# Kernel tuning notes

Measured on AMD Instinct MI355X. Metric: run time of the kernel, lower is better.

The kernel has to match this reference:

```python
import jax, jax.numpy as jnp
import numpy as np

N_HEADS, N_LEVELS, N_POINTS = 8, 4, 4
D_MODEL, D_FFN = 256, 2048
NQ, BS = 900, 4
SPATIAL = np.array([[128, 128], [64, 64], [32, 32], [16, 16]], dtype=np.int64)
HW = int((SPATIAL[:, 0] * SPATIAL[:, 1]).sum())


def _ln(x, g, b):
    mu = x.mean(-1, keepdims=True)
    var = x.var(-1, keepdims=True)
    return (x - mu) / jnp.sqrt(var + 1e-5) * g + b


def _lin(x, w, b):
    return x @ w.T + b


def _msdeform_attn(query, refp, mem, ss, starts, so_w, so_b, aw_w, aw_b, vp_w, vp_b, op_w, op_b):
    # query: (bs, nq, d), refp: (bs, nq, L, 2) in [0,1], mem: (bs, hw, d)
    bs, nq, d = query.shape
    hd = d // N_HEADS
    value = _lin(mem, vp_w, vp_b).reshape(bs, -1, N_HEADS, hd)  # (bs, hw, H, hd)
    offsets = _lin(query, so_w, so_b).reshape(bs, nq, N_HEADS, N_LEVELS, N_POINTS, 2)
    aw = _lin(query, aw_w, aw_b).reshape(bs, nq, N_HEADS, N_LEVELS * N_POINTS)
    aw = jax.nn.softmax(aw, axis=-1).reshape(bs, nq, N_HEADS, N_LEVELS, N_POINTS)
    # offset normalizer is (W, H) per level
    normalizer = jnp.asarray(ss[:, ::-1].copy(), dtype=query.dtype)  # (L, 2)
    loc = refp[:, :, None, :, None, :] + offsets / normalizer[None, None, None, :, None, :]
    out = jnp.zeros((bs, nq, N_HEADS, hd), dtype=query.dtype)
    for l in range(N_LEVELS):
        h_l, w_l = int(ss[l, 0]), int(ss[l, 1])
        vl = value[:, starts[l]:starts[l] + h_l * w_l]  # (bs, h*w, H, hd)
        # grid_sample align_corners=False: pixel coord = loc*size - 0.5
        x = loc[:, :, :, l, :, 0] * w_l - 0.5  # (bs, nq, H, P)
        y = loc[:, :, :, l, :, 1] * h_l - 0.5
        x0 = jnp.floor(x)
        y0 = jnp.floor(y)
        fx = x - x0
        fy = y - y0

        def gather(ix, iy, wgt):
            valid = (ix >= 0) & (ix < w_l) & (iy >= 0) & (iy < h_l)
            idx = (jnp.clip(iy, 0, h_l - 1) * w_l + jnp.clip(ix, 0, w_l - 1)).astype(jnp.int32)
            # (bs, nq, H, P) -> (bs, nq*P, H) to match vl's (bs, hw, H, hd)
            idxt = idx.transpose(0, 1, 3, 2).reshape(bs, nq * N_POINTS, N_HEADS)
            g = jnp.take_along_axis(vl, idxt[..., None], axis=1)  # (bs, nq*P, H, hd)
            g = g.reshape(bs, nq, N_POINTS, N_HEADS, hd).transpose(0, 1, 3, 2, 4)
            return g * (wgt * valid)[..., None]

        x0i = x0.astype(jnp.int32)
        y0i = y0.astype(jnp.int32)
        sampled = (gather(x0i, y0i, (1 - fx) * (1 - fy))
                   + gather(x0i + 1, y0i, fx * (1 - fy))
                   + gather(x0i, y0i + 1, (1 - fx) * fy)
                   + gather(x0i + 1, y0i + 1, fx * fy))  # (bs, nq, H, P, hd)
        out = out + (sampled * aw[:, :, :, l, :, None]).sum(axis=3)
    return _lin(out.reshape(bs, nq, d), op_w, op_b)


def _fwd(tgt, query_pos, memory, ref_points,
         sa_in_w, sa_in_b, sa_out_w, sa_out_b,
         ln1_g, ln1_b, ln2_g, ln2_b, ln3_g, ln3_b,
         so_w, so_b, aw_w, aw_b, vp_w, vp_b, op_w, op_b,
         ff1_w, ff1_b, ff2_w, ff2_b, spatial_shapes, level_start_index):
    nq, bs, d = tgt.shape
    hd = d // N_HEADS
    ss = np.asarray(spatial_shapes)
    starts = np.asarray(level_start_index)
    # ---- self attention (q = k = tgt + pos, v = tgt) ----
    qk = tgt + query_pos
    q = _lin(qk, sa_in_w[:d], sa_in_b[:d]).reshape(nq, bs, N_HEADS, hd)
    k = _lin(qk, sa_in_w[d:2 * d], sa_in_b[d:2 * d]).reshape(nq, bs, N_HEADS, hd)
    v = _lin(tgt, sa_in_w[2 * d:], sa_in_b[2 * d:]).reshape(nq, bs, N_HEADS, hd)
    scores = jnp.einsum('qbhd,kbhd->bhqk', q, k) / np.sqrt(hd).astype(tgt.dtype)
    attn = jax.nn.softmax(scores, axis=-1)
    sa = jnp.einsum('bhqk,kbhd->qbhd', attn, v).reshape(nq, bs, d)
    sa = _lin(sa, sa_out_w, sa_out_b)
    tgt = _ln(tgt + sa, ln2_g, ln2_b)
    # ---- deformable cross attention ----
    ca = _msdeform_attn((tgt + query_pos).transpose(1, 0, 2),
                        ref_points.transpose(1, 0, 2, 3),
                        memory.transpose(1, 0, 2), ss, starts,
                        so_w, so_b, aw_w, aw_b, vp_w, vp_b, op_w, op_b)
    tgt = _ln(tgt + ca.transpose(1, 0, 2), ln1_g, ln1_b)
    # ---- FFN ----
    ff = _lin(jax.nn.relu(_lin(tgt, ff1_w, ff1_b)), ff2_w, ff2_b)
    return _ln(tgt + ff, ln3_g, ln3_b)


def setup_inputs() -> dict:
    key = jax.random.key(0)
    ks = iter(jax.random.split(key, 32))
    d, dffn = D_MODEL, D_FFN
    nofs = N_HEADS * N_LEVELS * N_POINTS
    w = lambda *s: jax.random.normal(next(ks), s, dtype=jnp.float32) * 0.02
    starts = np.concatenate([[0], np.cumsum(SPATIAL[:, 0] * SPATIAL[:, 1])[:-1]]).astype(np.int64)
    return {
        'tgt': jax.random.normal(next(ks), (NQ, BS, d), dtype=jnp.float32),
        'query_pos': jax.random.normal(next(ks), (NQ, BS, d), dtype=jnp.float32),
        'memory': jax.random.normal(next(ks), (HW, BS, d), dtype=jnp.float32),
        'ref_points': jax.random.uniform(next(ks), (NQ, BS, N_LEVELS, 2), dtype=jnp.float32),
        'sa_in_w': w(3 * d, d), 'sa_in_b': w(3 * d), 'sa_out_w': w(d, d), 'sa_out_b': w(d),
        'ln1_g': jnp.ones((d,)), 'ln1_b': jnp.zeros((d,)),
        'ln2_g': jnp.ones((d,)), 'ln2_b': jnp.zeros((d,)),
        'ln3_g': jnp.ones((d,)), 'ln3_b': jnp.zeros((d,)),
        'so_w': w(nofs * 2, d), 'so_b': jax.random.normal(next(ks), (nofs * 2,), dtype=jnp.float32) * 0.5,
        'aw_w': w(nofs, d), 'aw_b': w(nofs),
        'vp_w': w(d, d), 'vp_b': w(d), 'op_w': w(d, d), 'op_b': w(d),
        'ff1_w': w(dffn, d), 'ff1_b': w(dffn), 'ff2_w': w(d, dffn), 'ff2_b': w(d),
        'spatial_shapes': SPATIAL, 'level_start_index': starts,
    }


def reference(tgt, query_pos, memory, ref_points, sa_in_w, sa_in_b, sa_out_w, sa_out_b, ln1_g, ln1_b, ln2_g, ln2_b, ln3_g, ln3_b, so_w, so_b, aw_w, aw_b, vp_w, vp_b, op_w, op_b, ff1_w, ff1_b, ff2_w, ff2_b, spatial_shapes, level_start_index):
    return _fwd(tgt, query_pos, memory, ref_points, sa_in_w, sa_in_b, sa_out_w, sa_out_b,
                ln1_g, ln1_b, ln2_g, ln2_b, ln3_g, ln3_b, so_w, so_b, aw_w, aw_b,
                vp_w, vp_b, op_w, op_b, ff1_w, ff1_b, ff2_w, ff2_b,
                spatial_shapes, level_start_index)
```

## Files before the change

### kernel.cpp

```cpp
#include <hip/hip_runtime.h>
#include <hip/hip_bf16.h>

#define D_MODEL 256
#define N_HEADS 8
#define HD 32
#define NQ 900
#define BS 4
#define MROWS (NQ * BS)
#define HW_TOT 21760
#define VROWS (HW_TOT * BS)

typedef __attribute__((ext_vector_type(8))) short bf16x8;
typedef __attribute__((ext_vector_type(4))) float f32x4;

__device__ inline short f2b(float f) {
  union { __hip_bfloat16 h; short s; } u;
  u.h = __float2bfloat16(f);
  return u.s;
}
__device__ inline float bu2f(unsigned short u) {
  union { unsigned int i; float f; } c;
  c.i = ((unsigned int)u) << 16;
  return c.f;
}
__device__ inline bf16x8 bzero8() {
  bf16x8 v;
#pragma unroll
  for (int j = 0; j < 8; ++j) v[j] = 0;
  return v;
}
__device__ inline f32x4 fzero4() {
  f32x4 v;
#pragma unroll
  for (int j = 0; j < 4; ++j) v[j] = 0.f;
  return v;
}

#define GLL16(gsrc, ldst)                                                     \
  __builtin_amdgcn_global_load_lds(                                           \
      (__attribute__((address_space(1))) void*)(gsrc),                        \
      (__attribute__((address_space(3))) void*)(ldst), 16, 0, 0)

__global__ __launch_bounds__(256) void prep_all(const float* __restrict__ s0,
                                                const float* __restrict__ s1,
                                                const float* __restrict__ s2,
                                                const float* __restrict__ s3,
                                                const float* __restrict__ s4,
                                                const float* __restrict__ s5,
                                                const float* __restrict__ s6,
                                                const float* __restrict__ s7,
                                                short* __restrict__ dst,
                                                const float* __restrict__ tgt,
                                                const float* __restrict__ qpos,
                                                short* __restrict__ tgtb,
                                                short* __restrict__ qkb,
                                                const float* __restrict__ so_b,
                                                const float* __restrict__ aw_b,
                                                float* __restrict__ biasSOAW) {
  int i = blockIdx.x * 256 + threadIdx.x;
  if (i < 1540096) {
    const float* s; int off;
    if (i < 196608)      { s = s0; off = 0; }
    else if (i < 262144) { s = s1; off = 196608; }
    else if (i < 327680) { s = s2; off = 262144; }
    else if (i < 360448) { s = s3; off = 327680; }
    else if (i < 425984) { s = s4; off = 360448; }
    else if (i < 491520) { s = s5; off = 425984; }
    else if (i < 1015808){ s = s6; off = 491520; }
    else                 { s = s7; off = 1015808; }
    dst[i] = f2b(s[i - off]);
  } else {
    int j = i - 1540096;
    float t = tgt[j], p = qpos[j];
    tgtb[j] = f2b(t);
    qkb[j] = f2b(t + p);
    if (j < 384) biasSOAW[j] = (j < 256) ? so_b[j] : aw_b[j - 256];
  }
}

template <int BN, int AF32, int OUTF32, int RELU>
__device__ __forceinline__ void gemm_core(const void* __restrict__ Xv,
                                          const short* __restrict__ W,
                                          const float* __restrict__ bias,
                                          void* __restrict__ outv,
                                          int M, int N, int K, int m0, int n0,
                                          int t0, int t1, int addBias,
                                          short* __restrict__ smem) {
  constexpr int NF = BN / 16;
  short* sA = smem;
  short* sB = smem + 2 * 2048;
  const int tid = threadIdx.x;
  const int wave = tid >> 6, lane = tid & 63;
  const int l15 = lane & 15, l4 = lane >> 4;
  const int wr = wave * 16;
  const float* Xf = (const float*)Xv;
  const short* Xh = (const short*)Xv;

  f32x4 acc[NF];
#pragma unroll
  for (int f = 0; f < NF; ++f) acc[f] = fzero4();

  const int alr = wave * 16 + (lane >> 2);
  const int ags = (lane & 3) ^ ((alr >> 1) & 3);
  const int arow = tid >> 2, ak = tid & 3;
  const int agsrc = ak ^ ((arow >> 1) & 3);
  float4 ra0, ra1;

  auto stageB = [&](int t, int buf) {
    short* bb = sB + buf * BN * 32;
#pragma unroll
    for (int j = 0; j < BN / 64; ++j) {
      int lr = j * 64 + alr;
      int gs = (lane & 3) ^ ((lr >> 1) & 3);
      const short* src = W + (size_t)(n0 + lr) * K + t * 32 + gs * 8;
      GLL16(src, bb + (j * 64 + wave * 16) * 32);
    }
  };
  auto stageA_gll = [&](int t, int buf) {
    const short* src = Xh + (size_t)(m0 + alr) * K + t * 32 + ags * 8;
    GLL16(src, sA + buf * 2048 + wave * 512);
  };
  auto loadA_f32 = [&](int t) {
    const float* p = Xf + (size_t)(m0 + arow) * K + t * 32 + agsrc * 8;
    ra0 = *reinterpret_cast<const float4*>(p);
    ra1 = *reinterpret_cast<const float4*>(p + 4);
  };
  auto writeA_f32 = [&](int buf) {
    bf16x8 v;
    v[0] = f2b(ra0.x); v[1] = f2b(ra0.y); v[2] = f2b(ra0.z); v[3] = f2b(ra0.w);
    v[4] = f2b(ra1.x); v[5] = f2b(ra1.y); v[6] = f2b(ra1.z); v[7] = f2b(ra1.w);
    *reinterpret_cast<bf16x8*>(&sA[buf * 2048 + arow * 32 + ak * 8]) = v;
  };
  auto compute = [&](int buf) {
    const int r = wr + l15;
    bf16x8 av = *reinterpret_cast<const bf16x8*>(
        &sA[buf * 2048 + r * 32 + ((l4 ^ ((r >> 1) & 3)) * 8)]);
#pragma unroll
    for (int f = 0; f < NF; ++f) {
      const int rb = f * 16 + l15;
      bf16x8 bv = *reinterpret_cast<const bf16x8*>(
          &sB[buf * BN * 32 + rb * 32 + ((l4 ^ ((rb >> 1) & 3)) * 8)]);
      acc[f] = __builtin_amdgcn_mfma_f32_16x16x32_bf16(av, bv, acc[f], 0, 0, 0);
    }
  };

  if constexpr (AF32) { loadA_f32(t0); writeA_f32(0); }
  else stageA_gll(t0, 0);
  stageB(t0, 0);
  __syncthreads();

  int buf = 0;
  for (int t = t0; t < t1; ++t) {
    if (t + 1 < t1) {
      if constexpr (AF32) loadA_f32(t + 1);
      else stageA_gll(t + 1, buf ^ 1);
      stageB(t + 1, buf ^ 1);
    }
    compute(buf);
    if (AF32 && t + 1 < t1) writeA_f32(buf ^ 1);
    __syncthreads();
    buf ^= 1;
  }

#pragma unroll
  for (int f = 0; f < NF; ++f) {
    int col = n0 + f * 16 + l15;
    float bfv = addBias ? bias[col] : 0.f;
#pragma unroll
    for (int i = 0; i < 4; ++i) {
      int row = m0 + wr + l4 * 4 + i;
      if (row >= M) continue;
      float v = acc[f][i] + bfv;
      if (RELU) v = fmaxf(v, 0.f);
      if constexpr (OUTF32)
        ((float*)outv)[(size_t)row * N + col] = v;
      else
        ((short*)outv)[(size_t)row * N + col] = f2b(v);
    }
  }
}

template <int BN, int AF32, int OUTF32, int RELU>
__global__ __launch_bounds__(256) void gemm2(const void* __restrict__ Xv,
                                             const short* __restrict__ W,
                                             const float* __restrict__ bias,
                                             void* __restrict__ outv,
                                             int M, int N, int K) {
  __shared__ __align__(16) short smem[2 * 2048 + 2 * BN * 32];
  gemm_core<BN, AF32, OUTF32, RELU>(Xv, W, bias, outv, M, N, K,
                                    blockIdx.x * 64, blockIdx.y * BN,
                                    0, K / 32, 1, smem);
}

__global__ __launch_bounds__(256) void gemm_splitk(const void* __restrict__ Xv,
                                                   const short* __restrict__ W,
                                                   const float* __restrict__ bias,
                                                   float* __restrict__ outp,
                                                   int M, int N, int K) {
  __shared__ __align__(16) short smem[2 * 2048 + 2 * 64 * 32];
  const int kc = blockIdx.z;
  const int ntc = K / 32 / 4;
  gemm_core<64, 0, 1, 0>(Xv, W, bias, outp + (size_t)kc * M * N, M, N, K,
                         blockIdx.x * 64, blockIdx.y * 64,
                         kc * ntc, (kc + 1) * ntc, kc == 0, smem);
}

__global__ __launch_bounds__(256) void qkv_gemm(const short* __restrict__ qkb,
                                                const short* __restrict__ tgtb,
                                                const short* __restrict__ Wqkv,
                                                const float* __restrict__ sa_in_b,
                                                short* __restrict__ QKb,
                                                short* __restrict__ Vb) {
  __shared__ __align__(16) short smem[2 * 2048 + 2 * 64 * 32];
  int bx = blockIdx.x;
  if (bx < 456) {
    gemm_core<64, 0, 0, 0>(qkb, Wqkv, sa_in_b, QKb, MROWS, 512, 256,
                           (bx % 57) * 64, (bx / 57) * 64, 0, 8, 1, smem);
  } else {
    bx -= 456;
    gemm_core<64, 0, 0, 0>(tgtb, Wqkv + 512 * 256, sa_in_b + 512, Vb, MROWS, 256, 256,
                           (bx % 57) * 64, (bx / 57) * 64, 0, 8, 1, smem);
  }
}

__device__ __forceinline__ void flash_body(const short* __restrict__ QK,
                                           const short* __restrict__ V,
                                           short* __restrict__ O,
                                           int bid, short* __restrict__ smem) {
  const int bh = bid & 31, b = bh >> 3, h = bh & 7;
  const int q0 = (bid >> 5) * 64;
  const int tid = threadIdx.x, wave = tid >> 6, lane = tid & 63;
  const int l15 = lane & 15, l4 = lane >> 4;
  const int cb = h * 32;

  short* sQ = smem;
  short* sK = smem + 2048;
  short* sVt = smem + 6144;
  short* sP = smem + 10752;

  const int sr = wave * 16 + (lane >> 2);
  const int sgs = (lane & 3) ^ (sr & 3);

  auto stageK = [&](int kt, int buf) {
    const short* src = QK + (size_t)((kt * 64 + sr) * 4 + b) * 512 + 256 + cb + sgs * 8;
    GLL16(src, sK + buf * 2048 + wave * 512);
  };
  const int vrow = tid >> 2, vdof = (tid & 3) * 8;
  const int vkp = vrow ^ (((vdof >> 3) & 3) << 4);
  auto loadV = [&](int kt) -> bf16x8 {
    int kk = kt * 64 + vrow;
    return (kk < NQ)
        ? *reinterpret_cast<const bf16x8*>(V + (size_t)(kk * 4 + b) * 256 + cb + vdof)
        : bzero8();
  };
  auto writeV = [&](bf16x8 vv, int buf) {
    short* dst = sVt + buf * 2304;
#pragma unroll
    for (int j = 0; j < 8; ++j) dst[(vdof + j) * 72 + vkp] = vv[j];
  };

  {
    const short* qsrc = QK + (size_t)((q0 + sr) * 4 + b) * 512 + cb + sgs * 8;
    GLL16(qsrc, sQ + wave * 512);
  }
  stageK(0, 0);
  {
    bf16x8 v0 = loadV(0);
    writeV(v0, 0);
  }
  __syncthreads();

  const int wr = wave * 16;
  const int rq = wr + l15;
  const bf16x8 aq = *reinterpret_cast<const bf16x8*>(&sQ[rq * 32 + ((l4 ^ (rq & 3)) * 8)]);

  float mrow[4], lrow[4];
#pragma unroll
  for (int i = 0; i < 4; ++i) { mrow[i] = -1e30f; lrow[i] = 0.f; }
  f32x4 accO[2];
  accO[0] = fzero4(); accO[1] = fzero4();

  const int pswz = (((wr >> 2) + l4) & 3) << 3;
  const int pswzr = (((wr >> 2) + (l15 >> 2)) & 3) << 3;

  for (int kt = 0; kt < 15; ++kt) {
    const int k0 = kt * 64;
    const int buf = kt & 1;
    const bool more = (kt + 1 < 15);
    bf16x8 vnext = bzero8();
    if (more) {
      stageK(kt + 1, buf ^ 1);
      vnext = loadV(kt + 1);
    }

    f32x4 s[4];
#pragma unroll
    for (int f = 0; f < 4; ++f) {
      const int rb = f * 16 + l15;
      bf16x8 bk = *reinterpret_cast<bf16x8*>(
          &sK[buf * 2048 + rb * 32 + ((l4 ^ (rb & 3)) * 8)]);
      s[f] = __builtin_amdgcn_mfma_f32_16x16x32_bf16(aq, bk, fzero4(), 0, 0, 0);
    }
#pragma unroll
    for (int f = 0; f < 4; ++f) {
      bool valid = (k0 + f * 16 + l15) < NQ;
#pragma unroll
      for (int i = 0; i < 4; ++i) {
        float sv = s[f][i] * 0.17677669529663687f;
        s[f][i] = valid ? sv : -1e30f;
      }
    }
    float mx[4];
#pragma unroll
    for (int i = 0; i < 4; ++i)
      mx[i] = fmaxf(fmaxf(s[0][i], s[1][i]), fmaxf(s[2][i], s[3][i]));
#pragma unroll
    for (int off = 1; off < 16; off <<= 1)
#pragma unroll
      for (int i = 0; i < 4; ++i) mx[i] = fmaxf(mx[i], __shfl_xor(mx[i], off));

    float alpha[4], rs[4];
#pragma unroll
    for (int i = 0; i < 4; ++i) {
      float mn = fmaxf(mrow[i], mx[i]);
      alpha[i] = __expf(mrow[i] - mn);
      mrow[i] = mn;
      rs[i] = 0.f;
    }
#pragma unroll
    for (int f = 0; f < 4; ++f)
#pragma unroll
      for (int i = 0; i < 4; ++i) {
        float p = __expf(s[f][i] - mrow[i]);
        rs[i] += p;
        sP[(wr + l4 * 4 + i) * 72 + ((f * 16 + l15) ^ pswz)] = f2b(p);
      }
#pragma unroll
    for (int off = 1; off < 16; off <<= 1)
#pragma unroll
      for (int i = 0; i < 4; ++i) rs[i] += __shfl_xor(rs[i], off);
#pragma unroll
    for (int i = 0; i < 4; ++i) lrow[i] = lrow[i] * alpha[i] + rs[i];
#pragma unroll
    for (int nf = 0; nf < 2; ++nf)
#pragma unroll
      for (int i = 0; i < 4; ++i) accO[nf][i] *= alpha[i];

#pragma unroll
    for (int ks = 0; ks < 2; ++ks) {
      bf16x8 ap = *reinterpret_cast<bf16x8*>(
          &sP[(wr + l15) * 72 + ((ks * 32 + l4 * 8) ^ pswzr)]);
#pragma unroll
      for (int nf = 0; nf < 2; ++nf) {
        const int d = nf * 16 + l15;
        const int kb = (ks * 32 + l4 * 8) ^ (((d >> 3) & 3) << 4);
        bf16x8 bv = *reinterpret_cast<bf16x8*>(&sVt[buf * 2304 + d * 72 + kb]);
        accO[nf] = __builtin_amdgcn_mfma_f32_16x16x32_bf16(ap, bv, accO[nf], 0, 0, 0);
      }
    }
    if (more) writeV(vnext, buf ^ 1);
    __syncthreads();
  }

#pragma unroll
  for (int nf = 0; nf < 2; ++nf)
#pragma unroll
    for (int i = 0; i < 4; ++i) {
      int q = q0 + wr + l4 * 4 + i;
      if (q < NQ)
        O[(size_t)(q * 4 + b) * 256 + cb + nf * 16 + l15] = f2b(accO[nf][i] / lrow[i]);
    }
}

__device__ __forceinline__ void value_core(const float* __restrict__ memory,
                                           const short* __restrict__ W,
                                           const float* __restrict__ vp_b,
                                           short* __restrict__ value, int vb,
                                           short* __restrict__ smem) {
  float* sAf = (float*)smem;
  short* sB = smem + 8192;
  const int tid = threadIdx.x;
  const int wave = tid >> 6, lane = tid & 63;
  const int l15 = lane & 15, l4 = lane >> 4;
  const int wr = wave * 16;
  const int m0 = (((vb >> 4) << 3) | (vb & 7)) * 64;
  const int n0 = ((vb >> 3) & 1) * 128;

  const int ar0 = wave * 16 + (lane >> 3);
  const int ag = (lane & 7) ^ (lane >> 3);
  auto stageA = [&](int t, int buf) {
    const float* s0 = memory + (size_t)(m0 + ar0) * 256 + t * 32 + ag * 4;
    GLL16(s0, (short*)sAf + buf * 4096 + wave * 1024);
    const float* s1 = memory + (size_t)(m0 + ar0 + 8) * 256 + t * 32 + ag * 4;
    GLL16(s1, (short*)sAf + buf * 4096 + wave * 1024 + 512);
  };
  const int blr = wave * 16 + (lane >> 2);
  auto stageB = [&](int t, int buf) {
#pragma unroll
    for (int j = 0; j < 2; ++j) {
      int lr = j * 64 + blr;
      int gs = (lane & 3) ^ ((lr >> 1) & 3);
      const short* src = W + (size_t)(n0 + lr) * 256 + t * 32 + gs * 8;
      GLL16(src, sB + buf * 4096 + (j * 64 + wave * 16) * 32);
    }
  };

  f32x4 acc[8];
#pragma unroll
  for (int f = 0; f < 8; ++f) acc[f] = fzero4();

  auto compute = [&](int buf) {
    const int r = wr + l15;
    const int rx = r & 7;
    const float* ap = sAf + buf * 2048 + r * 32;
    float4 a0 = *reinterpret_cast<const float4*>(ap + (((2 * l4) ^ rx) * 4));
    float4 a1 = *reinterpret_cast<const float4*>(ap + (((2 * l4 + 1) ^ rx) * 4));
    bf16x8 av;
    av[0] = f2b(a0.x); av[1] = f2b(a0.y); av[2] = f2b(a0.z); av[3] = f2b(a0.w);
    av[4] = f2b(a1.x); av[5] = f2b(a1.y); av[6] = f2b(a1.z); av[7] = f2b(a1.w);
#pragma unroll
    for (int f = 0; f < 8; ++f) {
      const int rb = f * 16 + l15;
      bf16x8 bv = *reinterpret_cast<const bf16x8*>(
          &sB[buf * 4096 + rb * 32 + ((l4 ^ ((rb >> 1) & 3)) * 8)]);
      acc[f] = __builtin_amdgcn_mfma_f32_16x16x32_bf16(av, bv, acc[f], 0, 0, 0);
    }
  };

  stageA(0, 0); stageB(0, 0);
  stageA(1, 1); stageB(1, 1);
  asm volatile("s_waitcnt vmcnt(4)" ::: "memory");
  __builtin_amdgcn_sched_barrier(0);
  __builtin_amdgcn_s_barrier();
  __builtin_amdgcn_sched_barrier(0);

#pragma unroll
  for (int t = 0; t < 8; ++t) {
    const int buf = t & 1;
    compute(buf);
    asm volatile("s_waitcnt lgkmcnt(0)" ::: "memory");
    __builtin_amdgcn_sched_barrier(0);
    __builtin_amdgcn_s_barrier();
    __builtin_amdgcn_sched_barrier(0);
    if (t + 2 < 8) { stageA(t + 2, buf); stageB(t + 2, buf); }
    if (t + 1 < 8) {
      if (t + 2 < 8) asm volatile("s_waitcnt vmcnt(4)" ::: "memory");
      else           asm volatile("s_waitcnt vmcnt(0)" ::: "memory");
      __builtin_amdgcn_sched_barrier(0);
      __builtin_amdgcn_s_barrier();
      __builtin_amdgcn_sched_barrier(0);
    }
  }

#pragma unroll
  for (int f = 0; f < 8; ++f) {
    const int col = n0 + f * 16 + l15;
    const float bb = vp_b[col];
#pragma unroll
    for (int i = 0; i < 4; ++i)
      value[(size_t)(m0 + wr + l4 * 4 + i) * 256 + col] = f2b(acc[f][i] + bb);
  }
}

__global__ __launch_bounds__(256) void flash_value(const short* __restrict__ QKb,
                                                   const short* __restrict__ Vb,
                                                   short* __restrict__ Ob,
                                                   const float* __restrict__ memory,
                                                   const short* __restrict__ Wvp,
                                                   const float* __restrict__ vp_b,
                                                   short* __restrict__ value) {
  __shared__ __align__(16) short smem[16384];
  int bx = blockIdx.x;
  if (bx < 480) {
    flash_body(QKb, Vb, Ob, bx, smem);
  } else {
    value_core(memory, Wvp, vp_b, value, bx - 480, smem);
  }
}

__global__ __launch_bounds__(256) void ln_kernel(const float* __restrict__ A,
                                                 const float* __restrict__ B,
                                                 const float* __restrict__ g,
                                                 const float* __restrict__ bb,
                                                 float* __restrict__ outF,
                                                 short* __restrict__ outB,
                                                 const float* __restrict__ addv) {
  const int row = blockIdx.x;
  const int t = threadIdx.x;
  const size_t base = (size_t)row * D_MODEL;
  float x = A[base + t] + B[base + t];
  float s = x, s2 = x * x;
#pragma unroll
  for (int off = 32; off; off >>= 1) {
    s += __shfl_xor(s, off);
    s2 += __shfl_xor(s2, off);
  }
  __shared__ float wsum[4], wsum2[4];
  const int w = t >> 6;
  if ((t & 63) == 0) { wsum[w] = s; wsum2[w] = s2; }
  __syncthreads();
  s = wsum[0] + wsum[1] + wsum[2] + wsum[3];
  s2 = wsum2[0] + wsum2[1] + wsum2[2] + wsum2[3];
  const float mu = s * (1.f / 256.f);
  const float var = s2 * (1.f / 256.f) - mu * mu;
  const float inv = rsqrtf(var + 1e-5f);
  float y = (x - mu) * inv * g[t] + bb[t];
  outF[base + t] = y;
  if (outB) outB[base + t] = f2b(y + (addv ? addv[base + t] : 0.f));
}

__global__ __launch_bounds__(256) void ln4_kernel(const float* __restrict__ A,
                                                  const float* __restrict__ P,
                                                  const float* __restrict__ g,
                                                  const float* __restrict__ bb,
                                                  float* __restrict__ outF) {
  const int row = blockIdx.x;
  const int t = threadIdx.x;
  const size_t base = (size_t)row * D_MODEL + t;
  const size_t stride = (size_t)MROWS * D_MODEL;
  float x = A[base] + P[base] + P[base + stride] + P[base + 2 * stride] + P[base + 3 * stride];
  float s = x, s2 = x * x;
#pragma unroll
  for (int off = 32; off; off >>= 1) {
    s += __shfl_xor(s, off);
    s2 += __shfl_xor(s2, off);
  }
  __shared__ float wsum[4], wsum2[4];
  const int w = t >> 6;
  if ((t & 63) == 0) { wsum[w] = s; wsum2[w] = s2; }
  __syncthreads();
  s = wsum[0] + wsum[1] + wsum[2] + wsum[3];
  s2 = wsum2[0] + wsum2[1] + wsum2[2] + wsum2[3];
  const float mu = s * (1.f / 256.f);
  const float var = s2 * (1.f / 256.f) - mu * mu;
  const float inv = rsqrtf(var + 1e-5f);
  outF[base] = (x - mu) * inv * g[t] + bb[t];
}

__global__ __launch_bounds__(256) void msds_kernel(const unsigned short* __restrict__ value,
                                                   const float* __restrict__ soaw,
                                                   const float* __restrict__ refp,
                                                   unsigned short* __restrict__ out) {
  const int tid = threadIdx.x;
  const int row = blockIdx.x * 8 + (tid >> 5);
  const int lane32 = tid & 31;
  const int h = lane32 >> 2;
  const int dp = (lane32 & 3) * 8;
  const int b = row & 3;

  const int WL[4] = {128, 64, 32, 16};
  const int ST[4] = {0, 16384, 20480, 21504};

  const float* awp = soaw + (size_t)row * 384 + 256 + h * 16;
  float awv[16];
  float m = -1e30f;
#pragma unroll
  for (int i = 0; i < 16; ++i) { awv[i] = awp[i]; m = fmaxf(m, awv[i]); }
  float s = 0.f;
#pragma unroll
  for (int i = 0; i < 16; ++i) { awv[i] = __expf(awv[i] - m); s += awv[i]; }
  const float invs = 1.f / s;

  const float* offp = soaw + (size_t)row * 384 + h * 32;
  float acc[8];
#pragma unroll
  for (int j = 0; j < 8; ++j) acc[j] = 0.f;

#pragma unroll
  for (int l = 0; l < 4; ++l) {
    const int wl = WL[l], hl = WL[l], st = ST[l];
    const float rx = refp[((size_t)row * 4 + l) * 2 + 0];
    const float ry = refp[((size_t)row * 4 + l) * 2 + 1];
#pragma unroll
    for (int p = 0; p < 4; ++p) {
      const float ox = offp[l * 8 + p * 2 + 0];
      const float oy = offp[l * 8 + p * 2 + 1];
      const float x = (rx + ox / (float)wl) * (float)wl - 0.5f;
      const float y = (ry + oy / (float)hl) * (float)hl - 0.5f;
      const float x0f = floorf(x), y0f = floorf(y);
      const int x0 = (int)x0f, y0 = (int)y0f;
      const float fx = x - x0f, fy = y - y0f;
      const float a = awv[l * 4 + p] * invs;
      const float w00 = (1.f - fx) * (1.f - fy);
      const float w10 = fx * (1.f - fy);
      const float w01 = (1.f - fx) * fy;
      const float w11 = fx * fy;
      float sv[8];
#pragma unroll
      for (int j = 0; j < 8; ++j) sv[j] = 0.f;
      auto gat = [&](int ix, int iy, float wgt) {
        if (ix >= 0 && ix < wl && iy >= 0 && iy < hl) {
          const unsigned short* p2 =
              value + ((size_t)((st + iy * wl + ix) * 4 + b)) * 256 + h * 32 + dp;
          bf16x8 u = *reinterpret_cast<const bf16x8*>(p2);
#pragma unroll
          for (int j = 0; j < 8; ++j) sv[j] += wgt * bu2f((unsigned short)u[j]);
        }
      };
      gat(x0, y0, w00);
      gat(x0 + 1, y0, w10);
      gat(x0, y0 + 1, w01);
      gat(x0 + 1, y0 + 1, w11);
#pragma unroll
      for (int j = 0; j < 8; ++j) acc[j] += a * sv[j];
    }
  }
  bf16x8 o;
#pragma unroll
  for (int j = 0; j < 8; ++j) o[j] = f2b(acc[j]);
  *reinterpret_cast<bf16x8*>(&out[(size_t)row * 256 + h * 32 + dp]) = o;
}

extern "C" void kernel_launch(void* const* d_in, const int* in_sizes, int n_in,
                              void* d_out, int out_size, void* d_ws, size_t ws_size,
                              hipStream_t stream) {
  const float* tgt      = (const float*)d_in[0];
  const float* qpos     = (const float*)d_in[1];
  const float* memory   = (const float*)d_in[2];
  const float* refp     = (const float*)d_in[3];
  const float* sa_in_w  = (const float*)d_in[4];
  const float* sa_in_b  = (const float*)d_in[5];
  const float* sa_out_w = (const float*)d_in[6];
  const float* sa_out_b = (const float*)d_in[7];
  const float* ln1_g = (const float*)d_in[8];
  const float* ln1_b = (const float*)d_in[9];
  const float* ln2_g = (const float*)d_in[10];
  const float* ln2_b = (const float*)d_in[11];
  const float* ln3_g = (const float*)d_in[12];
  const float* ln3_b = (const float*)d_in[13];
  const float* so_w = (const float*)d_in[14];
  const float* so_b = (const float*)d_in[15];
  const float* aw_w = (const float*)d_in[16];
  const float* aw_b = (const float*)d_in[17];
  const float* vp_w = (const float*)d_in[18];
  const float* vp_b = (const float*)d_in[19];
  const float* op_w = (const float*)d_in[20];
  const float* op_b = (const float*)d_in[21];
  const float* ff1_w = (const float*)d_in[22];
  const float* ff1_b = (const float*)d_in[23];
  const float* ff2_w = (const float*)d_in[24];
  const float* ff2_b = (const float*)d_in[25];

  float* out = (float*)d_out;
  float* ws = (float*)d_ws;

  short* Wb       = (short*)ws;
  float* biasSOAW = ws + 770048;
  short* tgtb   = (short*)(ws + 770432);
  short* qkb    = (short*)(ws + 1231232);
  short* QKb    = (short*)(ws + 1692032);
  short* Vb     = (short*)(ws + 2613632);
  short* Ob     = (short*)(ws + 3074432);
  float* SA     = ws + 3535232;
  float* F      = ws + 4456832;
  short* qk2b   = (short*)(ws + 5378432);
  float* SOAW   = ws + 5839232;
  short* value  = (short*)(ws + 7221632);
  short* sampled= (short*)(ws + 18362752);
  float* CA     = ws + 18823552;
  float* tgt3   = ws + 19745152;
  short* tgt3b  = (short*)(ws + 20666752);
  short* H      = (short*)(ws + 21127552);
  float* FFp    = ws + 7221632;

  const short* Wqkv = Wb;
  const short* Wsa  = Wb + 196608;
  const short* Wso  = Wb + 262144;
  const short* Wvp  = Wb + 360448;
  const short* Wop  = Wb + 425984;
  const short* Wff1 = Wb + 491520;
  const short* Wff2 = Wb + 1015808;

  prep_all<<<9616, 256, 0, stream>>>(sa_in_w, sa_out_w, so_w, aw_w, vp_w, op_w,
                                     ff1_w, ff2_w, Wb, tgt, qpos, tgtb, qkb,
                                     so_b, aw_b, biasSOAW);
  qkv_gemm<<<684, 256, 0, stream>>>(qkb, tgtb, Wqkv, sa_in_b, QKb, Vb);
  flash_value<<<3200, 256, 0, stream>>>(QKb, Vb, Ob, memory, Wvp, vp_b, value);
  gemm2<64, 0, 1, 0><<<dim3(57, 4), 256, 0, stream>>>(Ob, Wsa, sa_out_b, SA, MROWS, 256, 256);
  ln_kernel<<<MROWS, 256, 0, stream>>>(tgt, SA, ln2_g, ln2_b, F, qk2b, qpos);
  gemm2<64, 0, 1, 0><<<dim3(57, 6), 256, 0, stream>>>(qk2b, Wso, biasSOAW, SOAW, MROWS, 384, 256);
  msds_kernel<<<450, 256, 0, stream>>>((const unsigned short*)value, SOAW, refp,
                                       (unsigned short*)sampled);
  gemm2<64, 0, 1, 0><<<dim3(57, 4), 256, 0, stream>>>(sampled, Wop, op_b, CA, MROWS, 256, 256);
  ln_kernel<<<MROWS, 256, 0, stream>>>(F, CA, ln1_g, ln1_b, tgt3, tgt3b, nullptr);
  gemm2<64, 0, 0, 1><<<dim3(57, 32), 256, 0, stream>>>(tgt3b, Wff1, ff1_b, H, MROWS, 2048, 256);
  gemm_splitk<<<dim3(57, 4, 4), 256, 0, stream>>>(H, Wff2, ff2_b, FFp, MROWS, 256, 2048);
  ln4_kernel<<<MROWS, 256, 0, stream>>>(tgt3, FFp, ln3_g, ln3_b, out);
}
```

Baseline: 161.4 us.

## Fuse output-projection GEMMs with residual LayerNorm; triple-buffer value projection

Adds a gemm_ln kernel that computes a full 256-column row tile per block, adds bias and residual, and applies LayerNorm in registers. It replaces the two gemm2 + ln_kernel pairs, which removes two launches and the fp32 intermediate round trips through global memory. The cost is a grid of only 57 blocks, so most CUs sit idle during these GEMMs. Separately, the value-projection path in flash_value now uses three pipeline stages instead of two, which raises shared memory per block to 48KB and may lower occupancy for the flash blocks.

New measurement: 195.4 us. 21.1% more time.

```diff
diff --git a/kernel.cpp b/kernel.cpp
--- a/kernel.cpp
+++ b/kernel.cpp
@@ -205,6 +205,113 @@
                          kc * ntc, (kc + 1) * ntc, kc == 0, smem);
 }
 
+__global__ __launch_bounds__(256) void gemm_ln(const short* __restrict__ X,
+                                               const short* __restrict__ W,
+                                               const float* __restrict__ bias,
+                                               const float* __restrict__ R,
+                                               const float* __restrict__ g,
+                                               const float* __restrict__ bvec,
+                                               float* __restrict__ outF,
+                                               short* __restrict__ outB,
+                                               const float* __restrict__ addv) {
+  __shared__ __align__(16) short smem[2 * 2048 + 2 * 8192];
+  short* sA = smem;
+  short* sB = smem + 2 * 2048;
+  const int tid = threadIdx.x;
+  const int wave = tid >> 6, lane = tid & 63;
+  const int l15 = lane & 15, l4 = lane >> 4;
+  const int wr = wave * 16;
+  const int m0 = blockIdx.x * 64;
+
+  f32x4 acc[16];
+#pragma unroll
+  for (int f = 0; f < 16; ++f) acc[f] = fzero4();
+
+  const int alr = wave * 16 + (lane >> 2);
+  const int ags = (lane & 3) ^ ((alr >> 1) & 3);
+
+  auto stageA = [&](int t, int buf) {
+    const short* src = X + (size_t)(m0 + alr) * 256 + t * 32 + ags * 8;
+    GLL16(src, sA + buf * 2048 + wave * 512);
+  };
+  auto stageB = [&](int t, int buf) {
+#pragma unroll
+    for (int j = 0; j < 4; ++j) {
+      int lr = j * 64 + alr;
+      int gs = (lane & 3) ^ ((lr >> 1) & 3);
+      const short* src = W + (size_t)lr * 256 + t * 32 + gs * 8;
+      GLL16(src, sB + buf * 8192 + (j * 64 + wave * 16) * 32);
+    }
+  };
+  auto compute = [&](int buf) {
+    const int r = wr + l15;
+    bf16x8 av = *reinterpret_cast<const bf16x8*>(
+        &sA[buf * 2048 + r * 32 + ((l4 ^ ((r >> 1) & 3)) * 8)]);
+#pragma unroll
+    for (int f = 0; f < 16; ++f) {
+      const int rb = f * 16 + l15;
+      bf16x8 bv = *reinterpret_cast<const bf16x8*>(
+          &sB[buf * 8192 + rb * 32 + ((l4 ^ ((rb >> 1) & 3)) * 8)]);
+      acc[f] = __builtin_amdgcn_mfma_f32_16x16x32_bf16(av, bv, acc[f], 0, 0, 0);
+    }
+  };
+
+  stageA(0, 0); stageB(0, 0);
+  __syncthreads();
+  int buf = 0;
+  for (int t = 0; t < 8; ++t) {
+    if (t + 1 < 8) { stageA(t + 1, buf ^ 1); stageB(t + 1, buf ^ 1); }
+    compute(buf);
+    __syncthreads();
+    buf ^= 1;
+  }
+
+  float sum[4] = {0.f, 0.f, 0.f, 0.f}, sum2[4] = {0.f, 0.f, 0.f, 0.f};
+#pragma unroll
+  for (int f = 0; f < 16; ++f) {
+    const int col = f * 16 + l15;
+    const float bc = bias[col];
+#pragma unroll
+    for (int i = 0; i < 4; ++i) {
+      const int row = m0 + wr + l4 * 4 + i;
+      float r = (row < MROWS) ? R[(size_t)row * 256 + col] : 0.f;
+      float v = acc[f][i] + bc + r;
+      acc[f][i] = v;
+      sum[i] += v;
+      sum2[i] += v * v;
+    }
+  }
+#pragma unroll
+  for (int off = 1; off < 16; off <<= 1)
+#pragma unroll
+    for (int i = 0; i < 4; ++i) {
+      sum[i] += __shfl_xor(sum[i], off);
+      sum2[i] += __shfl_xor(sum2[i], off);
+    }
+  float mu[4], inv[4];
+#pragma unroll
+  for (int i = 0; i < 4; ++i) {
+    mu[i] = sum[i] * (1.f / 256.f);
+    float var = sum2[i] * (1.f / 256.f) - mu[i] * mu[i];
+    inv[i] = rsqrtf(var + 1e-5f);
+  }
+#pragma unroll
+  for (int f = 0; f < 16; ++f) {
+    const int col = f * 16 + l15;
+    const float gc = g[col], bc = bvec[col];
+#pragma unroll
+    for (int i = 0; i < 4; ++i) {
+      const int row = m0 + wr + l4 * 4 + i;
+      if (row >= MROWS) continue;
+      float y = (acc[f][i] - mu[i]) * inv[i] * gc + bc;
+      outF[(size_t)row * 256 + col] = y;
+      if (outB)
+        outB[(size_t)row * 256 + col] =
+            f2b(y + (addv ? addv[(size_t)row * 256 + col] : 0.f));
+    }
+  }
+}
+
 __global__ __launch_bounds__(256) void qkv_gemm(const short* __restrict__ qkb,
                                                 const short* __restrict__ tgtb,
                                                 const short* __restrict__ Wqkv,
@@ -378,7 +485,7 @@
                                            short* __restrict__ value, int vb,
                                            short* __restrict__ smem) {
   float* sAf = (float*)smem;
-  short* sB = smem + 8192;
+  short* sB = smem + 12288;
   const int tid = threadIdx.x;
   const int wave = tid >> 6, lane = tid & 63;
   const int l15 = lane & 15, l4 = lane >> 4;
@@ -429,23 +536,25 @@
 
   stageA(0, 0); stageB(0, 0);
   stageA(1, 1); stageB(1, 1);
-  asm volatile("s_waitcnt vmcnt(4)" ::: "memory");
+  stageA(2, 2); stageB(2, 2);
+  asm volatile("s_waitcnt vmcnt(8)" ::: "memory");
   __builtin_amdgcn_sched_barrier(0);
   __builtin_amdgcn_s_barrier();
   __builtin_amdgcn_sched_barrier(0);
 
 #pragma unroll
   for (int t = 0; t < 8; ++t) {
-    const int buf = t & 1;
+    const int buf = t % 3;
     compute(buf);
     asm volatile("s_waitcnt lgkmcnt(0)" ::: "memory");
     __builtin_amdgcn_sched_barrier(0);
     __builtin_amdgcn_s_barrier();
     __builtin_amdgcn_sched_barrier(0);
-    if (t + 2 < 8) { stageA(t + 2, buf); stageB(t + 2, buf); }
+    if (t + 3 < 8) { stageA(t + 3, buf); stageB(t + 3, buf); }
     if (t + 1 < 8) {
-      if (t + 2 < 8) asm volatile("s_waitcnt vmcnt(4)" ::: "memory");
-      else           asm volatile("s_waitcnt vmcnt(0)" ::: "memory");
+      if (t + 3 < 8)      asm volatile("s_waitcnt vmcnt(8)" ::: "memory");
+      else if (t + 2 < 8) asm volatile("s_waitcnt vmcnt(4)" ::: "memory");
+      else                asm volatile("s_waitcnt vmcnt(0)" ::: "memory");
       __builtin_amdgcn_sched_barrier(0);
       __builtin_amdgcn_s_barrier();
       __builtin_amdgcn_sched_barrier(0);
@@ -469,7 +578,7 @@
                                                    const short* __restrict__ Wvp,
                                                    const float* __restrict__ vp_b,
                                                    short* __restrict__ value) {
-  __shared__ __align__(16) short smem[16384];
+  __shared__ __align__(16) short smem[24576];
   int bx = blockIdx.x;
   if (bx < 480) {
     flash_body(QKb, Vb, Ob, bx, smem);
@@ -676,13 +785,13 @@
                                      so_b, aw_b, biasSOAW);
   qkv_gemm<<<684, 256, 0, stream>>>(qkb, tgtb, Wqkv, sa_in_b, QKb, Vb);
   flash_value<<<3200, 256, 0, stream>>>(QKb, Vb, Ob, memory, Wvp, vp_b, value);
-  gemm2<64, 0, 1, 0><<<dim3(57, 4), 256, 0, stream>>>(Ob, Wsa, sa_out_b, SA, MROWS, 256, 256);
-  ln_kernel<<<MROWS, 256, 0, stream>>>(tgt, SA, ln2_g, ln2_b, F, qk2b, qpos);
+  gemm_ln<<<57, 256, 0, stream>>>(Ob, Wsa, sa_out_b, tgt, ln2_g, ln2_b,
+                                  F, qk2b, qpos);
   gemm2<64, 0, 1, 0><<<dim3(57, 6), 256, 0, stream>>>(qk2b, Wso, biasSOAW, SOAW, MROWS, 384, 256);
   msds_kernel<<<450, 256, 0, stream>>>((const unsigned short*)value, SOAW, refp,
                                        (unsigned short*)sampled);
-  gemm2<64, 0, 1, 0><<<dim3(57, 4), 256, 0, stream>>>(sampled, Wop, op_b, CA, MROWS, 256, 256);
-  ln_kernel<<<MROWS, 256, 0, stream>>>(F, CA, ln1_g, ln1_b, tgt3, tgt3b, nullptr);
+  gemm_ln<<<57, 256, 0, stream>>>(sampled, Wop, op_b, F, ln1_g, ln1_b,
+                                  tgt3, tgt3b, nullptr);
   gemm2<64, 0, 0, 1><<<dim3(57, 32), 256, 0, stream>>>(tgt3b, Wff1, ff1_b, H, MROWS, 2048, 256);
   gemm_splitk<<<dim3(57, 4, 4), 256, 0, stream>>>(H, Wff2, ff2_b, FFp, MROWS, 256, 2048);
   ln4_kernel<<<MROWS, 256, 0, stream>>>(tgt3, FFp, ln3_g, ln3_b, out);
```
